# Kernel optimization log

Measured on AMD Instinct MI355X. Metric: run time of the kernel, lower is better.

The kernel has to match this reference:

```python
import jax, jax.numpy as jnp
import numpy as np

ROUTING_ITERS = 3

def _squash(s, axis=-1):
    # v = s * ||s||^2 / (1 + ||s||^2) / ||s||
    n2 = jnp.sum(s * s, axis=axis, keepdims=True)
    return s * n2 / (1.0 + n2) / jnp.sqrt(n2 + 1e-8)

def setup_inputs() -> dict:
    key = jax.random.key(0)
    k1, k2, k3 = jax.random.split(key, 3)
    B, R, C, O, I = 256, 1152, 10, 16, 8
    x = jax.random.normal(k1, (B, R, I), dtype=jnp.float32)
    W = jax.random.normal(k2, (R, C, O, I), dtype=jnp.float32) * 0.05
    bias = jax.random.normal(k3, (C, O), dtype=jnp.float32) * 0.05
    return {"x": x, "W": W, "bias": bias}

def reference(x, W, bias):
    # x: [B,R,I], W: [R,C,O,I], bias: [C,O]
    B = x.shape[0]
    R, C, O, I = W.shape
    # u_hat[b,r,c,o] = W[r,c,o,:] . x[b,r,:]   (torch: matmul(W, x) over broadcast batch)
    u_hat = jnp.einsum('rcoi,bri->brco', W, x)  # [B,R,C,O]
    b_ij = jnp.zeros((R, C), dtype=x.dtype)
    v = None
    for it in range(ROUTING_ITERS):
        c_ij = jax.nn.softmax(b_ij, axis=1)  # softmax over capsules (dim=2 in torch layout)
        s = jnp.einsum('rc,brco->bco', c_ij, u_hat) + bias  # [B,C,O]
        v = _squash(s, axis=-1)  # squash over out_channels (dim=-2 of [B,1,C,O,1])
        if it < ROUTING_ITERS - 1:
            # agreement: u_hat^T v, then mean over batch (keepdim collapses to shared logits)
            agree = jnp.einsum('brco,bco->brc', u_hat, v).mean(axis=0)  # [R,C]
            b_ij = b_ij + agree
    # torch returns v_j.squeeze(1): [B, C, O, 1]
    return v[..., None]
```

## Files before the change

### kernel.cpp

```cpp
#include <hip/hip_runtime.h>

#define CB 256
#define CR 1152
#define CC 10
#define CO 16
#define CI 8
#define CK (CR*CI)
#define NCO (CC*CO)

typedef __bf16 bf16_t;
typedef __attribute__((ext_vector_type(8))) __bf16 bf16x8;
typedef __attribute__((ext_vector_type(4))) float f32x4;

__global__ __launch_bounds__(256) void k_cvt(const float* __restrict__ x,
                                             const float* __restrict__ W,
                                             bf16_t* __restrict__ xb,
                                             bf16_t* __restrict__ xTb,
                                             bf16_t* __restrict__ Wt) {
  const int t = threadIdx.x;
  if (blockIdx.x < 1152) {
    const int bt = blockIdx.x & 7, kt = blockIdx.x >> 3;
    const int b0 = bt * 32, k0 = kt * 64;
    __shared__ float ldsT[64][33];
    const int row = t >> 3, cv = t & 7;
    const float4* xp = (const float4*)(x + (size_t)(b0 + row) * CK + k0 + cv * 8);
    const float4 f0 = xp[0], f1 = xp[1];
    float vals[8] = {f0.x, f0.y, f0.z, f0.w, f1.x, f1.y, f1.z, f1.w};
    bf16x8 ov;
    #pragma unroll
    for (int j = 0; j < 8; ++j) {
      ov[j] = (bf16_t)vals[j];
      ldsT[cv * 8 + j][row] = vals[j];
    }
    *(bf16x8*)(xb + (size_t)(b0 + row) * CK + k0 + cv * 8) = ov;
    __syncthreads();
    const int kr = t >> 2, bs = t & 3;
    bf16x8 tv;
    #pragma unroll
    for (int j = 0; j < 8; ++j) tv[j] = (bf16_t)ldsT[kr][bs * 8 + j];
    *(bf16x8*)(xTb + (size_t)(k0 + kr) * CB + b0 + bs * 8) = tv;
  } else {
    const int wi = (blockIdx.x - 1152) * 256 + t;
    const int r = wi % CR;
    const int co = wi / CR;
    const int c = co >> 4, o = co & 15;
    const float4* src = (const float4*)(W + (((size_t)r * CC + c) * CO + o) * CI);
    const float4 f0 = src[0], f1 = src[1];
    bf16x8 v;
    v[0] = (bf16_t)f0.x; v[1] = (bf16_t)f0.y; v[2] = (bf16_t)f0.z; v[3] = (bf16_t)f0.w;
    v[4] = (bf16_t)f1.x; v[5] = (bf16_t)f1.y; v[6] = (bf16_t)f1.z; v[7] = (bf16_t)f1.w;
    *(bf16x8*)(Wt + (size_t)co * CK + r * 8) = v;
  }
}

template<int MODE, bool LAST>
__global__ __launch_bounds__(512) void k_s(const bf16_t* __restrict__ xb,
                                           const bf16_t* __restrict__ Bmat,
                                           const float* __restrict__ bias,
                                           bf16_t* __restrict__ vTb,
                                           float* __restrict__ out) {
  const int bt = blockIdx.x, c = blockIdx.y;
  const int t = threadIdx.x;
  const int w = t >> 6, lane = t & 63;
  const int mrow = lane & 15, kg = lane >> 4;
  const int b0 = bt * 16;
  const size_t kbase = (size_t)w * (CK / 8);

  const bf16x8* ap = (const bf16x8*)(xb + (size_t)(b0 + mrow) * CK + kbase) + kg;
  const bf16x8* bp = (const bf16x8*)(Bmat + (size_t)(c * CO + mrow) * CK + kbase) + kg;

  f32x4 acc0 = {0.f, 0.f, 0.f, 0.f}, acc1 = {0.f, 0.f, 0.f, 0.f};
  #pragma unroll 6
  for (int s = 0; s < 36; s += 2) {
    acc0 = __builtin_amdgcn_mfma_f32_16x16x32_bf16(ap[s * 4], bp[s * 4], acc0, 0, 0, 0);
    acc1 = __builtin_amdgcn_mfma_f32_16x16x32_bf16(ap[(s + 1) * 4], bp[(s + 1) * 4], acc1, 0, 0, 0);
  }
  const f32x4 acc = acc0 + acc1;

  __shared__ float Ls[8][64][4];
  #pragma unroll
  for (int reg = 0; reg < 4; ++reg) Ls[w][lane][reg] = acc[reg];
  __syncthreads();

  if (t < 256) {
    const int row = t >> 4, col = t & 15;
    const int l = ((row >> 2) << 4) | col, reg = row & 3;
    float s = 0.f;
    #pragma unroll
    for (int q = 0; q < 8; ++q) s += Ls[q][l][reg];
    if (MODE == 0) s *= 0.1f;
    s += bias[c * CO + col];
    float n2 = s * s;
    #pragma unroll
    for (int m = 1; m < 16; m <<= 1) n2 += __shfl_xor(n2, m);
    const float vv = s * n2 / (1.f + n2) * rsqrtf(n2 + 1e-8f);
    if (LAST) out[(size_t)(b0 + row) * NCO + c * CO + col] = vv;
    else      vTb[(size_t)(c * CO + col) * CB + b0 + row] = (bf16_t)vv;
  }
}

template<bool FIRST>
__global__ __launch_bounds__(256) void k_asc(const bf16_t* __restrict__ xTb,
                                             const bf16_t* __restrict__ vTb,
                                             const float* __restrict__ W,
                                             const bf16_t* __restrict__ Wt,
                                             float* __restrict__ b_ij,
                                             bf16_t* __restrict__ Wts) {
  const int r0 = blockIdx.x * 8;
  const int t = threadIdx.x;
  const int w = t >> 6, lane = t & 63;
  const int mrow = lane & 15, kg = lane >> 4;

  __shared__ __align__(16) unsigned short vL[NCO][CB + 8];
  __shared__ float agrL[8][CC];
  __shared__ float cwL[8][CC];

  #pragma unroll
  for (int q = 0; q < 20; ++q) {
    const int idx = q * 256 + t;
    const int co = idx >> 5, bs = idx & 31;
    const bf16x8 v = ((const bf16x8*)vTb)[idx];
    *(bf16x8*)&vL[co][bs * 8] = v;
  }

  const int m0 = r0 * 8 + w * 16;
  const bf16x8* ap = (const bf16x8*)(xTb + (size_t)(m0 + mrow) * CB) + kg;
  bf16x8 a[8];
  #pragma unroll
  for (int s = 0; s < 8; ++s) a[s] = ap[s * 4];
  __syncthreads();

  const int o = lane & 15, g = lane >> 4;
  for (int c = 0; c < CC; ++c) {
    f32x4 acc = {0.f, 0.f, 0.f, 0.f};
    #pragma unroll
    for (int s = 0; s < 8; ++s) {
      const bf16x8 bv = *(const bf16x8*)&vL[c * CO + mrow][s * 32 + kg * 8];
      acc = __builtin_amdgcn_mfma_f32_16x16x32_bf16(a[s], bv, acc, 0, 0, 0);
    }
    float p = 0.f;
    #pragma unroll
    for (int reg = 0; reg < 4; ++reg) {
      const int m = g * 4 + reg, rl = m >> 3, i = m & 7;
      p += acc[reg] * W[(((size_t)(r0 + w * 2 + rl) * CC + c) * CO + o) * CI + i];
    }
    #pragma unroll
    for (int msk = 1; msk < 32; msk <<= 1) p += __shfl_xor(p, msk);
    if ((lane & 31) == 0) agrL[w * 2 + (lane >> 5)][c] = p * (1.0f / CB);
  }
  __syncthreads();

  if (t < 8) {
    const int r = r0 + t;
    float nb[CC];
    float mx = -1e30f;
    #pragma unroll
    for (int c = 0; c < CC; ++c) {
      nb[c] = (FIRST ? 0.f : b_ij[r * CC + c]) + agrL[t][c];
      mx = fmaxf(mx, nb[c]);
    }
    float sum = 0.f;
    #pragma unroll
    for (int c = 0; c < CC; ++c) {
      b_ij[r * CC + c] = nb[c];
      const float e = __expf(nb[c] - mx);
      cwL[t][c] = e;
      sum += e;
    }
    const float inv = 1.f / sum;
    #pragma unroll
    for (int c = 0; c < CC; ++c) cwL[t][c] *= inv;
  }
  __syncthreads();

  #pragma unroll
  for (int q = 0; q < 5; ++q) {
    const int slot = q * 256 + t;
    const int co = slot >> 3, rl = slot & 7;
    const float cw = cwL[rl][co >> 4];
    const size_t off = (size_t)co * CK + (r0 + rl) * 8;
    const bf16x8 wv = *(const bf16x8*)(Wt + off);
    bf16x8 ov;
    #pragma unroll
    for (int j = 0; j < 8; ++j) ov[j] = (bf16_t)((float)wv[j] * cw);
    *(bf16x8*)(Wts + off) = ov;
  }
}

extern "C" void kernel_launch(void* const* d_in, const int* in_sizes, int n_in,
                              void* d_out, int out_size, void* d_ws, size_t ws_size,
                              hipStream_t stream) {
  const float* x    = (const float*)d_in[0];
  const float* W    = (const float*)d_in[1];
  const float* bias = (const float*)d_in[2];
  float* out = (float*)d_out;

  bf16_t* xb  = (bf16_t*)d_ws;
  bf16_t* xTb = xb  + (size_t)CB * CK;
  bf16_t* Wt  = xTb + (size_t)CB * CK;
  bf16_t* Wts = Wt  + (size_t)NCO * CK;
  bf16_t* vTb = Wts + (size_t)NCO * CK;
  float*  b_ij = (float*)(vTb + (size_t)NCO * CB);

  k_cvt<<<1872, 256, 0, stream>>>(x, W, xb, xTb, Wt);

  k_s<0, false><<<dim3(16, 10), 512, 0, stream>>>(xb, Wt, bias, vTb, out);
  k_asc<true><<<144, 256, 0, stream>>>(xTb, vTb, W, Wt, b_ij, Wts);

  k_s<1, false><<<dim3(16, 10), 512, 0, stream>>>(xb, Wts, bias, vTb, out);
  k_asc<false><<<144, 256, 0, stream>>>(xTb, vTb, W, Wt, b_ij, Wts);

  k_s<1, true><<<dim3(16, 10), 512, 0, stream>>>(xb, Wts, bias, vTb, out);
}
```

Before: 88.45 us.

## Fuse all routing stages into one persistent cooperative kernel with grid syncs

Replaces the six separate kernel launches (convert, three s/squash passes, two agreement/softmax passes) with a single cooperative kernel of 256 blocks that steps through the stages using grid.sync(). Routing logits b_ij now stay in shared memory per block instead of a global buffer, and the agreement stage splits the capsule loop across two half-blocks. The x transpose is rewritten as strided gathers without an LDS tile. This removes launch gaps and inter-kernel overhead but adds grid-wide barrier cost, leaves most blocks idle in each routing stage, and the uncoalesced transpose reads may be slower than the old LDS transpose.

```diff
diff --git a/kernel.cpp b/kernel.cpp
--- a/kernel.cpp
+++ b/kernel.cpp
@@ -1,4 +1,7 @@
 #include <hip/hip_runtime.h>
+#include <hip/hip_cooperative_groups.h>
+
+namespace cg = cooperative_groups;
 
 #define CB 256
 #define CR 1152
@@ -7,183 +10,186 @@
 #define CI 8
 #define CK (CR*CI)
 #define NCO (CC*CO)
+#define GRD 256
+#define THR 512
 
 typedef __bf16 bf16_t;
 typedef __attribute__((ext_vector_type(8))) __bf16 bf16x8;
 typedef __attribute__((ext_vector_type(4))) float f32x4;
 
-__global__ __launch_bounds__(256) void k_cvt(const float* __restrict__ x,
-                                             const float* __restrict__ W,
-                                             bf16_t* __restrict__ xb,
-                                             bf16_t* __restrict__ xTb,
-                                             bf16_t* __restrict__ Wt) {
-  const int t = threadIdx.x;
-  if (blockIdx.x < 1152) {
-    const int bt = blockIdx.x & 7, kt = blockIdx.x >> 3;
-    const int b0 = bt * 32, k0 = kt * 64;
-    __shared__ float ldsT[64][33];
-    const int row = t >> 3, cv = t & 7;
-    const float4* xp = (const float4*)(x + (size_t)(b0 + row) * CK + k0 + cv * 8);
-    const float4 f0 = xp[0], f1 = xp[1];
-    float vals[8] = {f0.x, f0.y, f0.z, f0.w, f1.x, f1.y, f1.z, f1.w};
-    bf16x8 ov;
-    #pragma unroll
-    for (int j = 0; j < 8; ++j) {
-      ov[j] = (bf16_t)vals[j];
-      ldsT[cv * 8 + j][row] = vals[j];
-    }
-    *(bf16x8*)(xb + (size_t)(b0 + row) * CK + k0 + cv * 8) = ov;
-    __syncthreads();
-    const int kr = t >> 2, bs = t & 3;
-    bf16x8 tv;
-    #pragma unroll
-    for (int j = 0; j < 8; ++j) tv[j] = (bf16_t)ldsT[kr][bs * 8 + j];
-    *(bf16x8*)(xTb + (size_t)(k0 + kr) * CB + b0 + bs * 8) = tv;
-  } else {
-    const int wi = (blockIdx.x - 1152) * 256 + t;
-    const int r = wi % CR;
-    const int co = wi / CR;
-    const int c = co >> 4, o = co & 15;
-    const float4* src = (const float4*)(W + (((size_t)r * CC + c) * CO + o) * CI);
-    const float4 f0 = src[0], f1 = src[1];
-    bf16x8 v;
-    v[0] = (bf16_t)f0.x; v[1] = (bf16_t)f0.y; v[2] = (bf16_t)f0.z; v[3] = (bf16_t)f0.w;
-    v[4] = (bf16_t)f1.x; v[5] = (bf16_t)f1.y; v[6] = (bf16_t)f1.z; v[7] = (bf16_t)f1.w;
-    *(bf16x8*)(Wt + (size_t)co * CK + r * 8) = v;
-  }
-}
-
-template<int MODE, bool LAST>
-__global__ __launch_bounds__(512) void k_s(const bf16_t* __restrict__ xb,
-                                           const bf16_t* __restrict__ Bmat,
-                                           const float* __restrict__ bias,
-                                           bf16_t* __restrict__ vTb,
-                                           float* __restrict__ out) {
-  const int bt = blockIdx.x, c = blockIdx.y;
-  const int t = threadIdx.x;
-  const int w = t >> 6, lane = t & 63;
-  const int mrow = lane & 15, kg = lane >> 4;
-  const int b0 = bt * 16;
-  const size_t kbase = (size_t)w * (CK / 8);
-
-  const bf16x8* ap = (const bf16x8*)(xb + (size_t)(b0 + mrow) * CK + kbase) + kg;
-  const bf16x8* bp = (const bf16x8*)(Bmat + (size_t)(c * CO + mrow) * CK + kbase) + kg;
-
-  f32x4 acc0 = {0.f, 0.f, 0.f, 0.f}, acc1 = {0.f, 0.f, 0.f, 0.f};
-  #pragma unroll 6
-  for (int s = 0; s < 36; s += 2) {
-    acc0 = __builtin_amdgcn_mfma_f32_16x16x32_bf16(ap[s * 4], bp[s * 4], acc0, 0, 0, 0);
-    acc1 = __builtin_amdgcn_mfma_f32_16x16x32_bf16(ap[(s + 1) * 4], bp[(s + 1) * 4], acc1, 0, 0, 0);
-  }
-  const f32x4 acc = acc0 + acc1;
-
-  __shared__ float Ls[8][64][4];
-  #pragma unroll
-  for (int reg = 0; reg < 4; ++reg) Ls[w][lane][reg] = acc[reg];
-  __syncthreads();
-
-  if (t < 256) {
-    const int row = t >> 4, col = t & 15;
-    const int l = ((row >> 2) << 4) | col, reg = row & 3;
-    float s = 0.f;
-    #pragma unroll
-    for (int q = 0; q < 8; ++q) s += Ls[q][l][reg];
-    if (MODE == 0) s *= 0.1f;
-    s += bias[c * CO + col];
-    float n2 = s * s;
-    #pragma unroll
-    for (int m = 1; m < 16; m <<= 1) n2 += __shfl_xor(n2, m);
-    const float vv = s * n2 / (1.f + n2) * rsqrtf(n2 + 1e-8f);
-    if (LAST) out[(size_t)(b0 + row) * NCO + c * CO + col] = vv;
-    else      vTb[(size_t)(c * CO + col) * CB + b0 + row] = (bf16_t)vv;
-  }
-}
-
-template<bool FIRST>
-__global__ __launch_bounds__(256) void k_asc(const bf16_t* __restrict__ xTb,
-                                             const bf16_t* __restrict__ vTb,
-                                             const float* __restrict__ W,
-                                             const bf16_t* __restrict__ Wt,
-                                             float* __restrict__ b_ij,
-                                             bf16_t* __restrict__ Wts) {
-  const int r0 = blockIdx.x * 8;
-  const int t = threadIdx.x;
-  const int w = t >> 6, lane = t & 63;
-  const int mrow = lane & 15, kg = lane >> 4;
-
-  __shared__ __align__(16) unsigned short vL[NCO][CB + 8];
+union SMem {
+  float Ls[8][64][4];
+  unsigned short vL[NCO][CB + 8];
+};
+
+__global__ __launch_bounds__(THR, 1) void k_fused(
+    const float* __restrict__ x, const float* __restrict__ W,
+    const float* __restrict__ bias, float* __restrict__ out,
+    bf16_t* __restrict__ xb, bf16_t* __restrict__ xTb,
+    bf16_t* __restrict__ Wt, bf16_t* __restrict__ Wts,
+    bf16_t* __restrict__ vTb) {
+  cg::grid_group grid = cg::this_grid();
+  __shared__ SMem sm;
+  __shared__ float bL[8][CC];
   __shared__ float agrL[8][CC];
   __shared__ float cwL[8][CC];
 
-  #pragma unroll
-  for (int q = 0; q < 20; ++q) {
-    const int idx = q * 256 + t;
-    const int co = idx >> 5, bs = idx & 31;
-    const bf16x8 v = ((const bf16x8*)vTb)[idx];
-    *(bf16x8*)&vL[co][bs * 8] = v;
+  const int blk = blockIdx.x;
+  const int t = threadIdx.x;
+
+  for (int job = blk; job < 1512; job += GRD) {
+    if (job < 576) {
+      const int vi = job * THR + t;
+      const float4 f0 = ((const float4*)x)[vi * 2];
+      const float4 f1 = ((const float4*)x)[vi * 2 + 1];
+      bf16x8 ov;
+      ov[0] = (bf16_t)f0.x; ov[1] = (bf16_t)f0.y; ov[2] = (bf16_t)f0.z; ov[3] = (bf16_t)f0.w;
+      ov[4] = (bf16_t)f1.x; ov[5] = (bf16_t)f1.y; ov[6] = (bf16_t)f1.z; ov[7] = (bf16_t)f1.w;
+      ((bf16x8*)xb)[vi] = ov;
+    } else if (job < 1152) {
+      const int u = (job - 576) * THR + t;
+      const int bg = u / 9216;
+      const int k = u - bg * 9216;
+      const int b0 = bg * 8;
+      bf16x8 tv;
+      #pragma unroll
+      for (int j = 0; j < 8; ++j) tv[j] = (bf16_t)x[(size_t)(b0 + j) * CK + k];
+      *(bf16x8*)(xTb + (size_t)k * CB + b0) = tv;
+    } else {
+      const int wi = (job - 1152) * THR + t;
+      const int r = wi % CR;
+      const int co = wi / CR;
+      const int c = co >> 4, o = co & 15;
+      const float4* src = (const float4*)(W + (((size_t)r * CC + c) * CO + o) * CI);
+      const float4 f0 = src[0], f1 = src[1];
+      bf16x8 v;
+      v[0] = (bf16_t)f0.x; v[1] = (bf16_t)f0.y; v[2] = (bf16_t)f0.z; v[3] = (bf16_t)f0.w;
+      v[4] = (bf16_t)f1.x; v[5] = (bf16_t)f1.y; v[6] = (bf16_t)f1.z; v[7] = (bf16_t)f1.w;
+      *(bf16x8*)(Wt + (size_t)co * CK + r * 8) = v;
+    }
   }
-
-  const int m0 = r0 * 8 + w * 16;
-  const bf16x8* ap = (const bf16x8*)(xTb + (size_t)(m0 + mrow) * CB) + kg;
-  bf16x8 a[8];
-  #pragma unroll
-  for (int s = 0; s < 8; ++s) a[s] = ap[s * 4];
-  __syncthreads();
-
-  const int o = lane & 15, g = lane >> 4;
-  for (int c = 0; c < CC; ++c) {
-    f32x4 acc = {0.f, 0.f, 0.f, 0.f};
-    #pragma unroll
-    for (int s = 0; s < 8; ++s) {
-      const bf16x8 bv = *(const bf16x8*)&vL[c * CO + mrow][s * 32 + kg * 8];
-      acc = __builtin_amdgcn_mfma_f32_16x16x32_bf16(a[s], bv, acc, 0, 0, 0);
+  grid.sync();
+
+  for (int it = 0; it < 3; ++it) {
+    if (blk < 160) {
+      const int bt = blk & 15, c = blk >> 4;
+      const int w = t >> 6, lane = t & 63;
+      const int mrow = lane & 15, kg = lane >> 4;
+      const int b0 = bt * 16;
+      const bf16_t* __restrict__ Bmat = (it == 0) ? Wt : Wts;
+      const size_t kbase = (size_t)w * (CK / 8);
+      const bf16x8* ap = (const bf16x8*)(xb + (size_t)(b0 + mrow) * CK + kbase) + kg;
+      const bf16x8* bp = (const bf16x8*)(Bmat + (size_t)(c * CO + mrow) * CK + kbase) + kg;
+      f32x4 acc0 = {0.f, 0.f, 0.f, 0.f}, acc1 = {0.f, 0.f, 0.f, 0.f};
+      #pragma unroll 6
+      for (int s = 0; s < 36; s += 2) {
+        acc0 = __builtin_amdgcn_mfma_f32_16x16x32_bf16(ap[s * 4], bp[s * 4], acc0, 0, 0, 0);
+        acc1 = __builtin_amdgcn_mfma_f32_16x16x32_bf16(ap[(s + 1) * 4], bp[(s + 1) * 4], acc1, 0, 0, 0);
+      }
+      const f32x4 acc = acc0 + acc1;
+      #pragma unroll
+      for (int reg = 0; reg < 4; ++reg) sm.Ls[w][lane][reg] = acc[reg];
+      __syncthreads();
+      if (t < 256) {
+        const int row = t >> 4, col = t & 15;
+        const int l = ((row >> 2) << 4) | col, reg = row & 3;
+        float s = 0.f;
+        #pragma unroll
+        for (int q = 0; q < 8; ++q) s += sm.Ls[q][l][reg];
+        if (it == 0) s *= 0.1f;
+        s += bias[c * CO + col];
+        float n2 = s * s;
+        #pragma unroll
+        for (int m = 1; m < 16; m <<= 1) n2 += __shfl_xor(n2, m);
+        const float vv = s * n2 / (1.f + n2) * rsqrtf(n2 + 1e-8f);
+        if (it == 2) out[(size_t)(b0 + row) * NCO + c * CO + col] = vv;
+        else         vTb[(size_t)(c * CO + col) * CB + b0 + row] = (bf16_t)vv;
+      }
     }
-    float p = 0.f;
-    #pragma unroll
-    for (int reg = 0; reg < 4; ++reg) {
-      const int m = g * 4 + reg, rl = m >> 3, i = m & 7;
-      p += acc[reg] * W[(((size_t)(r0 + w * 2 + rl) * CC + c) * CO + o) * CI + i];
+    grid.sync();
+    if (it == 2) break;
+
+    if (blk < 144) {
+      const int r0 = blk * 8;
+      const int h = t >> 8;
+      const int th = t & 255;
+      const int w = th >> 6, lane = th & 63;
+      const int mrow = lane & 15, kg = lane >> 4;
+
+      #pragma unroll
+      for (int q = 0; q < 10; ++q) {
+        const int idx = q * THR + t;
+        const int co = idx >> 5, bs = idx & 31;
+        const bf16x8 v = ((const bf16x8*)vTb)[idx];
+        *(bf16x8*)&sm.vL[co][bs * 8] = v;
+      }
+      const int m0 = r0 * 8 + w * 16;
+      const bf16x8* ap = (const bf16x8*)(xTb + (size_t)(m0 + mrow) * CB) + kg;
+      bf16x8 a[8];
+      #pragma unroll
+      for (int s = 0; s < 8; ++s) a[s] = ap[s * 4];
+      __syncthreads();
+
+      const int o = lane & 15, g = lane >> 4;
+      #pragma unroll
+      for (int cc = 0; cc < 5; ++cc) {
+        const int c = h * 5 + cc;
+        f32x4 acc = {0.f, 0.f, 0.f, 0.f};
+        #pragma unroll
+        for (int s = 0; s < 8; ++s) {
+          const bf16x8 bv = *(const bf16x8*)&sm.vL[c * CO + mrow][s * 32 + kg * 8];
+          acc = __builtin_amdgcn_mfma_f32_16x16x32_bf16(a[s], bv, acc, 0, 0, 0);
+        }
+        float p = 0.f;
+        #pragma unroll
+        for (int reg = 0; reg < 4; ++reg) {
+          const int m = g * 4 + reg, rl = m >> 3, i = m & 7;
+          p += acc[reg] * W[(((size_t)(r0 + w * 2 + rl) * CC + c) * CO + o) * CI + i];
+        }
+        #pragma unroll
+        for (int msk = 1; msk < 32; msk <<= 1) p += __shfl_xor(p, msk);
+        if ((lane & 31) == 0) agrL[w * 2 + (lane >> 5)][c] = p * (1.0f / CB);
+      }
+      __syncthreads();
+
+      if (t < 8) {
+        float nb[CC];
+        float mx = -1e30f;
+        #pragma unroll
+        for (int c = 0; c < CC; ++c) {
+          nb[c] = (it == 0 ? 0.f : bL[t][c]) + agrL[t][c];
+          mx = fmaxf(mx, nb[c]);
+        }
+        float sum = 0.f;
+        #pragma unroll
+        for (int c = 0; c < CC; ++c) {
+          bL[t][c] = nb[c];
+          const float e = __expf(nb[c] - mx);
+          cwL[t][c] = e;
+          sum += e;
+        }
+        const float inv = 1.f / sum;
+        #pragma unroll
+        for (int c = 0; c < CC; ++c) cwL[t][c] *= inv;
+      }
+      __syncthreads();
+
+      #pragma unroll
+      for (int q = 0; q < 3; ++q) {
+        const int slot = q * THR + t;
+        if (slot < 1280) {
+          const int co = slot >> 3, rl = slot & 7;
+          const float cw = cwL[rl][co >> 4];
+          const size_t off = (size_t)co * CK + (r0 + rl) * 8;
+          const bf16x8 wv = *(const bf16x8*)(Wt + off);
+          bf16x8 ov;
+          #pragma unroll
+          for (int j = 0; j < 8; ++j) ov[j] = (bf16_t)((float)wv[j] * cw);
+          *(bf16x8*)(Wts + off) = ov;
+        }
+      }
     }
-    #pragma unroll
-    for (int msk = 1; msk < 32; msk <<= 1) p += __shfl_xor(p, msk);
-    if ((lane & 31) == 0) agrL[w * 2 + (lane >> 5)][c] = p * (1.0f / CB);
-  }
-  __syncthreads();
-
-  if (t < 8) {
-    const int r = r0 + t;
-    float nb[CC];
-    float mx = -1e30f;
-    #pragma unroll
-    for (int c = 0; c < CC; ++c) {
-      nb[c] = (FIRST ? 0.f : b_ij[r * CC + c]) + agrL[t][c];
-      mx = fmaxf(mx, nb[c]);
-    }
-    float sum = 0.f;
-    #pragma unroll
-    for (int c = 0; c < CC; ++c) {
-      b_ij[r * CC + c] = nb[c];
-      const float e = __expf(nb[c] - mx);
-      cwL[t][c] = e;
-      sum += e;
-    }
-    const float inv = 1.f / sum;
-    #pragma unroll
-    for (int c = 0; c < CC; ++c) cwL[t][c] *= inv;
-  }
-  __syncthreads();
-
-  #pragma unroll
-  for (int q = 0; q < 5; ++q) {
-    const int slot = q * 256 + t;
-    const int co = slot >> 3, rl = slot & 7;
-    const float cw = cwL[rl][co >> 4];
-    const size_t off = (size_t)co * CK + (r0 + rl) * 8;
-    const bf16x8 wv = *(const bf16x8*)(Wt + off);
-    bf16x8 ov;
-    #pragma unroll
-    for (int j = 0; j < 8; ++j) ov[j] = (bf16_t)((float)wv[j] * cw);
-    *(bf16x8*)(Wts + off) = ov;
+    grid.sync();
   }
 }
 
@@ -200,15 +206,9 @@
   bf16_t* Wt  = xTb + (size_t)CB * CK;
   bf16_t* Wts = Wt  + (size_t)NCO * CK;
   bf16_t* vTb = Wts + (size_t)NCO * CK;
-  float*  b_ij = (float*)(vTb + (size_t)NCO * CB);
-
-  k_cvt<<<1872, 256, 0, stream>>>(x, W, xb, xTb, Wt);
-
-  k_s<0, false><<<dim3(16, 10), 512, 0, stream>>>(xb, Wt, bias, vTb, out);
-  k_asc<true><<<144, 256, 0, stream>>>(xTb, vTb, W, Wt, b_ij, Wts);
-
-  k_s<1, false><<<dim3(16, 10), 512, 0, stream>>>(xb, Wts, bias, vTb, out);
-  k_asc<false><<<144, 256, 0, stream>>>(xTb, vTb, W, Wt, b_ij, Wts);
-
-  k_s<1, true><<<dim3(16, 10), 512, 0, stream>>>(xb, Wts, bias, vTb, out);
+
+  void* args[] = {(void*)&x, (void*)&W, (void*)&bias, (void*)&out,
+                  (void*)&xb, (void*)&xTb, (void*)&Wt, (void*)&Wts, (void*)&vTb};
+  hipLaunchCooperativeKernel((const void*)k_fused, dim3(GRD), dim3(THR),
+                             args, 0, stream);
 }
```

Measured after the change: 284.8 us. +222.0%, slower.
